# Kernel optimization log

Measured on AMD Instinct MI355X. Metric: run time of the kernel, lower is better.

The kernel has to match this reference:

```python
import jax, jax.numpy as jnp
import numpy as np

B, N = 4, 1024
DIM, DEPTH, HEADS, DHEAD, MLP = 512, 6, 8, 64, 2048
INNER = HEADS * DHEAD
SCALE = DHEAD ** -0.5
EPS = 1e-5


def setup_inputs() -> dict:
    key = jax.random.key(0)
    ks = jax.random.split(key, 16)
    w = lambda k, shape: (jax.random.normal(k, shape, jnp.float32) * 0.02)
    D = DEPTH
    return {
        "g": jax.random.normal(ks[0], (B, N, DIM), jnp.float32),
        "x": jax.random.normal(ks[1], (B, N, DIM), jnp.float32),
        # PreNorm + SelfAttention
        "ln1_s": jnp.ones((D, DIM)), "ln1_b": jnp.zeros((D, DIM)),
        "Wqkv": w(ks[2], (D, DIM, 3 * INNER)),
        "Wo_sa": w(ks[3], (D, INNER, DIM)), "bo_sa": jnp.zeros((D, DIM)),
        # RelationalCrossAttention
        "lng_s": jnp.ones((D, DIM)), "lng_b": jnp.zeros((D, DIM)),
        "lnx_s": jnp.ones((D, DIM)), "lnx_b": jnp.zeros((D, DIM)),
        "Wq": w(ks[4], (D, DIM, INNER)),
        "Wk": w(ks[5], (D, DIM, INNER)),
        "Wv": w(ks[6], (D, DIM, INNER)), "bv": jnp.zeros((D, INNER)),
        "Wo_ca": w(ks[7], (D, INNER, DIM)), "bo_ca": jnp.zeros((D, DIM)),
        # PreNorm + FeedForward (same module applied twice per layer)
        "lnf_s": jnp.ones((D, DIM)), "lnf_b": jnp.zeros((D, DIM)),
        "W1": w(ks[8], (D, DIM, MLP)), "b1": jnp.zeros((D, MLP)),
        "W2": w(ks[9], (D, MLP, DIM)), "b2": jnp.zeros((D, DIM)),
    }


def _ln(t, s, b):
    m = t.mean(-1, keepdims=True)
    v = ((t - m) ** 2).mean(-1, keepdims=True)
    return (t - m) / jnp.sqrt(v + EPS) * s + b


def _split_heads(t):  # [b, n, h*d] -> [b, h, n, d]
    b, n, _ = t.shape
    return t.reshape(b, n, HEADS, DHEAD).transpose(0, 2, 1, 3)


def _merge_heads(t):  # [b, h, n, d] -> [b, n, h*d]
    b, h, n, d = t.shape
    return t.transpose(0, 2, 1, 3).reshape(b, n, h * d)


def _attend(q, k, v):
    dots = jnp.einsum('bhnd,bhmd->bhnm', q, k) * SCALE
    attn = jax.nn.softmax(jnp.nan_to_num(dots, nan=-jnp.inf), axis=-1)
    attn = jnp.nan_to_num(attn)  # nan_to_num(0.0) post-softmax as in source
    return jnp.einsum('bhnm,bhmd->bhnd', attn, jnp.nan_to_num(v))


def reference(g, x, ln1_s, ln1_b, Wqkv, Wo_sa, bo_sa, lng_s, lng_b, lnx_s, lnx_b,
              Wq, Wk, Wv, bv, Wo_ca, bo_ca, lnf_s, lnf_b, W1, b1, W2, b2):
    for i in range(DEPTH):
        def ff(t):
            h = jax.nn.gelu(_ln(t, lnf_s[i], lnf_b[i]) @ W1[i] + b1[i], approximate=False)
            return h @ W2[i] + b2[i]
        # relational cross attention: q,k from g, v from x
        gn = _ln(g, lng_s[i], lng_b[i])
        xn = _ln(x, lnx_s[i], lnx_b[i])
        q = _split_heads(gn @ Wq[i])
        k = _split_heads(gn @ Wk[i])
        v = _split_heads(xn @ Wv[i] + bv[i])
        x = _merge_heads(_attend(q, k, v)) @ Wo_ca[i] + bo_ca[i] + x
        x = ff(x) + x
        # pre-norm self attention (skip connection enabled)
        sn = _ln(x, ln1_s[i], ln1_b[i])
        qkv = sn @ Wqkv[i]
        qs, ks_, vs = jnp.split(qkv, 3, axis=-1)
        sa = _merge_heads(_attend(_split_heads(qs), _split_heads(ks_), _split_heads(vs)))
        x = sa @ Wo_sa[i] + bo_sa[i] + x
        x = ff(x) + x
    return x
```

## Files before the change

### kernel.cpp

```cpp
#include <hip/hip_runtime.h>
#include <hip/hip_bf16.h>
#include <cstdint>
#include <cstddef>

#define DEV __device__ __forceinline__

using f32x4 = __attribute__((ext_vector_type(4))) float;
using bfx8  = __attribute__((ext_vector_type(8))) __bf16;
using s16x8 = __attribute__((ext_vector_type(8))) short;

DEV uint16_t f2bf(float f) {
    union { float f; uint32_t u; } x; x.f = f;
    uint32_t r = x.u + 0x7fffu + ((x.u >> 16) & 1u);
    return (uint16_t)(r >> 16);
}

DEV float gelu_exact(float v) {
    return 0.5f * v * (1.0f + erff(v * 0.70710678118654752f));
}

DEV f32x4 mfma16(s16x8 a, s16x8 b, f32x4 c) {
    return __builtin_amdgcn_mfma_f32_16x16x32_bf16(
        __builtin_bit_cast(bfx8, a), __builtin_bit_cast(bfx8, b), c, 0, 0, 0);
}

DEV void async_lds16(const void* g, void* l) {
    __builtin_amdgcn_global_load_lds(
        (const __attribute__((address_space(1))) uint32_t*)g,
        (__attribute__((address_space(3))) uint32_t*)l, 16, 0, 0);
}

template<int N> DEV void wait_vmcnt() {
    if constexpr (N == 0)      asm volatile("s_waitcnt vmcnt(0)" ::: "memory");
    else if constexpr (N == 4) asm volatile("s_waitcnt vmcnt(4)" ::: "memory");
    else static_assert(N == 0 || N == 4, "add vmcnt literal");
}
#define SBAR      asm volatile("s_barrier" ::: "memory")
#define LGKM0     asm volatile("s_waitcnt lgkmcnt(0)" ::: "memory")
#define SCHED0    __builtin_amdgcn_sched_barrier(0)

template<int HAS_SB>
__global__ __launch_bounds__(256)
void ln_t(const float* __restrict__ in, const float* __restrict__ sc,
          const float* __restrict__ bi, uint16_t* __restrict__ out)
{
    const int lane = threadIdx.x & 63;
    const size_t row = (size_t)blockIdx.x * 4 + (threadIdx.x >> 6);
    const float* p = in + row * 512 + lane * 8;
    float4 a = *(const float4*)p;
    float4 b4 = *(const float4*)(p + 4);
    float v[8] = {a.x, a.y, a.z, a.w, b4.x, b4.y, b4.z, b4.w};
    float s = 0.f, sq = 0.f;
#pragma unroll
    for (int j = 0; j < 8; ++j) { s += v[j]; sq += v[j] * v[j]; }
#pragma unroll
    for (int o = 1; o < 64; o <<= 1) { s += __shfl_xor(s, o); sq += __shfl_xor(sq, o); }
    const float mean = s * (1.0f / 512.0f);
    const float var  = sq * (1.0f / 512.0f) - mean * mean;
    const float rstd = rsqrtf(var + 1e-5f);
    const int c = lane * 8;
    uint16_t o8[8];
#pragma unroll
    for (int j = 0; j < 8; ++j) {
        float z = (v[j] - mean) * rstd;
        if (HAS_SB) z = z * sc[c + j] + bi[c + j];
        o8[j] = f2bf(z);
    }
    uint4 pk;
    pk.x = (uint32_t)o8[0] | ((uint32_t)o8[1] << 16);
    pk.y = (uint32_t)o8[2] | ((uint32_t)o8[3] << 16);
    pk.z = (uint32_t)o8[4] | ((uint32_t)o8[5] << 16);
    pk.w = (uint32_t)o8[6] | ((uint32_t)o8[7] << 16);
    *reinterpret_cast<uint4*>(out + row * 512 + c) = pk;
}

__global__ __launch_bounds__(256)
void wtrans(const float* __restrict__ W, uint16_t* __restrict__ WT, int K, int N,
            size_t lstride, int row0, const float* __restrict__ kscale)
{
    __shared__ float tile[32][33];
    const int l = blockIdx.z;
    const int k0 = blockIdx.x * 32, n0 = blockIdx.y * 32;
    const float* Wl = W + (size_t)l * K * N;
    uint16_t* WTl = WT + (size_t)l * lstride;
    const int tx = threadIdx.x, ty = threadIdx.y;
#pragma unroll
    for (int j = 0; j < 4; ++j) {
        const int k = k0 + ty + j * 8;
        float w = Wl[(size_t)k * N + n0 + tx];
        if (kscale) w *= kscale[l * K + k];
        tile[ty + j * 8][tx] = w;
    }
    __syncthreads();
#pragma unroll
    for (int j = 0; j < 4; ++j)
        WTl[(size_t)(row0 + n0 + ty + j * 8) * K + k0 + tx] = f2bf(tile[tx][ty + j * 8]);
}

__global__ __launch_bounds__(256)
void bfold(const float* __restrict__ b, const float* __restrict__ Wq,
           const float* __restrict__ Wk, float* __restrict__ out)
{
    const int n = blockIdx.x * 256 + threadIdx.x;
    const int l = blockIdx.y, sel = blockIdx.z;
    const float* bb = b + l * 512;
    const float* W = (sel ? Wk : Wq) + (size_t)l * 512 * 512;
    float s = 0.f;
    for (int k = 0; k < 512; ++k) s += bb[k] * W[(size_t)k * 512 + n];
    out[l * 1024 + sel * 512 + n] = s;
}

template<int BM, int BN, int NWR, int NWC, int MINW,
         int HAS_BIAS, int HAS_RESID, int DO_GELU, int OUT_BF16, int PARTIAL, int OUT_VT>
__global__ __launch_bounds__(NWR * NWC * 64, MINW)
void gemm6(const uint16_t* __restrict__ A, const uint16_t* __restrict__ BT,
           const float* __restrict__ bias, const float* __restrict__ resid,
           void* __restrict__ outp, uint16_t* __restrict__ vt,
           int M, int N, int K, int kh)
{
    constexpr int NT = NWR * NWC * 64;
    constexpr int WM = BM / NWR, WN = BN / NWC;
    constexpr int FM = WM / 16, FN = WN / 16;
    constexpr int ASLOTS = 8 * BM, BSLOTS = 8 * BN, TOT = ASLOTS + BSLOTS;
    constexpr int S = TOT / NT;
    static_assert(S == 4, "vmcnt literal assumes S==4");
    __shared__ uint16_t As[2][ASLOTS * 8];
    __shared__ uint16_t Bs[2][BSLOTS * 8];
    const int tid = threadIdx.x, lane = tid & 63;
    const int w = tid >> 6, wr = w / NWC, wc = w % NWC;
    const int kg = lane >> 4, lr = lane & 15;
    const int nwg = gridDim.x;
    const int id0 = blockIdx.x;
    const int id = (id0 & 7) * (nwg >> 3) + (id0 >> 3);
    const int nbn = N / BN;
    const size_t m0 = (size_t)(id / nbn) * BM;
    const size_t n0 = (size_t)(id % nbn) * BN;
    const int kbase = PARTIAL ? blockIdx.y * kh : 0;

    auto stage = [&](int b, int k0) {
#pragma unroll
        for (int j = 0; j < S; ++j) {
            const int s = j * NT + tid;
            if (s < ASLOTS) {
                const int sub = s / BM, row = s % BM;
                async_lds16(A + (m0 + row) * K + k0 + sub * 8, &As[b][s * 8]);
            } else {
                const int s2 = s - ASLOTS;
                const int sub = s2 / BN, row = s2 % BN;
                async_lds16(BT + (n0 + row) * K + k0 + sub * 8, &Bs[b][s2 * 8]);
            }
        }
    };

    f32x4 acc[FM][FN] = {};
    const int nt = kh / 64;
    stage(0, kbase);
    stage(1, kbase + 64);
    int cur = 0;
    for (int t = 0; t < nt; ++t) {
        if (t < nt - 1) wait_vmcnt<S>(); else wait_vmcnt<0>();
        SBAR;
        s16x8 af[2][FM], bf[2][FN];
#pragma unroll
        for (int ks = 0; ks < 2; ++ks) {
#pragma unroll
            for (int i = 0; i < FM; ++i)
                af[ks][i] = *(const s16x8*)&As[cur][((ks * 4 + kg) * BM + wr * WM + i * 16 + lr) * 8];
#pragma unroll
            for (int j = 0; j < FN; ++j)
                bf[ks][j] = *(const s16x8*)&Bs[cur][((ks * 4 + kg) * BN + wc * WN + j * 16 + lr) * 8];
        }
        __builtin_amdgcn_s_setprio(1);
#pragma unroll
        for (int ks = 0; ks < 2; ++ks)
#pragma unroll
            for (int i = 0; i < FM; ++i)
#pragma unroll
                for (int j = 0; j < FN; ++j)
                    acc[i][j] = mfma16(af[ks][i], bf[ks][j], acc[i][j]);
        __builtin_amdgcn_s_setprio(0);
        LGKM0; SCHED0;
        SBAR;
        if (t + 2 < nt) stage(cur, kbase + (t + 2) * 64);
        cur ^= 1;
    }
    if (OUT_VT == 1 || (OUT_VT == 2 && n0 >= 1024)) {
#pragma unroll
        for (int i = 0; i < FM; ++i) {
            const size_t rbase = m0 + wr * WM + i * 16 + kg * 4;
            const int b = (int)(rbase >> 10), nloc = (int)(rbase & 1023);
#pragma unroll
            for (int j = 0; j < FN; ++j) {
                const int col = (int)n0 + wc * WN + j * 16 + lr;
                const int c2 = (OUT_VT == 2) ? col - 1024 : col;
                const float bval = HAS_BIAS ? bias[c2] : 0.0f;
                const int h = c2 >> 6, d = c2 & 63;
                ushort4 pk;
                pk.x = f2bf(acc[i][j][0] + bval);
                pk.y = f2bf(acc[i][j][1] + bval);
                pk.z = f2bf(acc[i][j][2] + bval);
                pk.w = f2bf(acc[i][j][3] + bval);
                *(ushort4*)&vt[((size_t)(b * 8 + h) * 64 + d) * 1024 + nloc] = pk;
            }
        }
        return;
    }
    float* pout = PARTIAL ? (float*)outp + (size_t)blockIdx.y * M * (size_t)N : nullptr;
#pragma unroll
    for (int i = 0; i < FM; ++i) {
        const size_t rbase = m0 + wr * WM + i * 16 + kg * 4;
#pragma unroll
        for (int j = 0; j < FN; ++j) {
            const size_t col = n0 + wc * WN + j * 16 + lr;
            const float bval = HAS_BIAS ? bias[col] : 0.0f;
#pragma unroll
            for (int r = 0; r < 4; ++r) {
                const size_t row = rbase + r;
                float v = acc[i][j][r] + bval;
                if (PARTIAL) { pout[row * (size_t)N + col] = v; continue; }
                if (DO_GELU)  v = gelu_exact(v);
                if (HAS_RESID) v += resid[row * (size_t)N + col];
                if (OUT_BF16) ((uint16_t*)outp)[row * (size_t)N + col] = f2bf(v);
                else          ((float*)outp)[row * (size_t)N + col] = v;
            }
        }
    }
}

template<int DO_LN>
__global__ __launch_bounds__(256)
void reduce_ln(const float* __restrict__ p, const float* __restrict__ bias,
               float* __restrict__ x, const float* __restrict__ sc,
               const float* __restrict__ bi, uint16_t* __restrict__ xn)
{
    const int lane = threadIdx.x & 63;
    const size_t row = (size_t)blockIdx.x * 4 + (threadIdx.x >> 6);
    const int c = lane * 8;
    const size_t off = row * 512 + c;
    const float* p0 = p + off;
    const float* p1 = p + 4096ull * 512 + off;
    float4 a0 = *(const float4*)p0,        a1 = *(const float4*)(p0 + 4);
    float4 b0 = *(const float4*)p1,        b1 = *(const float4*)(p1 + 4);
    float4 s0 = *(const float4*)(bias + c), s1 = *(const float4*)(bias + c + 4);
    float4 r0 = *(const float4*)(x + off), r1 = *(const float4*)(x + off + 4);
    float v[8];
    v[0] = a0.x + b0.x + s0.x + r0.x;  v[1] = a0.y + b0.y + s0.y + r0.y;
    v[2] = a0.z + b0.z + s0.z + r0.z;  v[3] = a0.w + b0.w + s0.w + r0.w;
    v[4] = a1.x + b1.x + s1.x + r1.x;  v[5] = a1.y + b1.y + s1.y + r1.y;
    v[6] = a1.z + b1.z + s1.z + r1.z;  v[7] = a1.w + b1.w + s1.w + r1.w;
    *(float4*)(x + off)     = make_float4(v[0], v[1], v[2], v[3]);
    *(float4*)(x + off + 4) = make_float4(v[4], v[5], v[6], v[7]);
    if (DO_LN) {
        float s = 0.f, sq = 0.f;
#pragma unroll
        for (int j = 0; j < 8; ++j) { s += v[j]; sq += v[j] * v[j]; }
#pragma unroll
        for (int o = 1; o < 64; o <<= 1) { s += __shfl_xor(s, o); sq += __shfl_xor(sq, o); }
        const float mean = s * (1.0f / 512.0f);
        const float var  = sq * (1.0f / 512.0f) - mean * mean;
        const float rstd = rsqrtf(var + 1e-5f);
        uint16_t o8[8];
#pragma unroll
        for (int j = 0; j < 8; ++j)
            o8[j] = f2bf((v[j] - mean) * rstd * sc[c + j] + bi[c + j]);
        uint4 pk;
        pk.x = (uint32_t)o8[0] | ((uint32_t)o8[1] << 16);
        pk.y = (uint32_t)o8[2] | ((uint32_t)o8[3] << 16);
        pk.z = (uint32_t)o8[4] | ((uint32_t)o8[5] << 16);
        pk.w = (uint32_t)o8[6] | ((uint32_t)o8[7] << 16);
        *reinterpret_cast<uint4*>(xn + off) = pk;
    }
}

__global__ __launch_bounds__(256)
void attn_flash(const uint16_t* __restrict__ Qb, const uint16_t* __restrict__ Kb,
                const uint16_t* __restrict__ Vt, uint16_t* __restrict__ Ob,
                int qstride, int kstride, int qoff, int koff)
{
    __shared__ uint16_t Ks[2][4096];
    __shared__ uint16_t Vs[2][4096];
    __shared__ uint16_t Pb[4][1024];
    const int tid = threadIdx.x, lane = tid & 63, w = tid >> 6;
    const int kg = lane >> 4, lr = lane & 15;
    const int bh = blockIdx.y, b = bh >> 3, h = bh & 7;
    const int q0 = blockIdx.x * 64;
    const float CEXP = 0.125f * 1.44269504f;

    s16x8 aq0, aq1;
    {
        const size_t qrow = (size_t)b * 1024 + q0 + w * 16 + lr;
        const uint16_t* qp = Qb + qrow * qstride + qoff + h * 64 + kg * 8;
        aq0 = *(const s16x8*)qp;
        aq1 = *(const s16x8*)(qp + 32);
    }
    const uint16_t* kbase = Kb + (size_t)b * 1024 * kstride + koff + h * 64;
    const uint16_t* vbase = Vt + (size_t)bh * 65536;

    float l_r[4] = {0.f, 0.f, 0.f, 0.f};
    f32x4 acc[4] = {};

    auto stage = [&](int buf, int kv0) {
#pragma unroll
        for (int j = 0; j < 2; ++j) {
            const int s = j * 256 + tid;
            const int sub = s >> 6, row = s & 63;
            async_lds16(kbase + (size_t)(kv0 + row) * kstride + sub * 8, &Ks[buf][s * 8]);
            async_lds16(vbase + (size_t)row * 1024 + kv0 + sub * 8,      &Vs[buf][s * 8]);
        }
    };

    stage(0, 0);
    __syncthreads();
    int cur = 0;
    for (int t = 0; t < 16; ++t) {
        if (t < 15) stage(cur ^ 1, (t + 1) * 64);
        f32x4 s4[4];
        __builtin_amdgcn_s_setprio(1);
#pragma unroll
        for (int ni = 0; ni < 4; ++ni) {
            s16x8 bk0 = *(const s16x8*)&Ks[cur][(kg * 64 + ni * 16 + lr) * 8];
            s16x8 bk1 = *(const s16x8*)&Ks[cur][((4 + kg) * 64 + ni * 16 + lr) * 8];
            f32x4 z = {};
            z = mfma16(aq0, bk0, z);
            z = mfma16(aq1, bk1, z);
            s4[ni] = z;
        }
        __builtin_amdgcn_s_setprio(0);
#pragma unroll
        for (int ni = 0; ni < 4; ++ni) {
            const int slotb = (ni * 2 + (lr >> 3)) * 16 + kg * 4;
#pragma unroll
            for (int r = 0; r < 4; ++r) {
                const float pe = __builtin_amdgcn_exp2f(s4[ni][r] * CEXP);
                l_r[r] += pe;
                Pb[w][(slotb + r) * 8 + (lr & 7)] = f2bf(pe);
            }
        }
        s16x8 ap0 = *(const s16x8*)&Pb[w][(kg * 16 + lr) * 8];
        s16x8 ap1 = *(const s16x8*)&Pb[w][((4 + kg) * 16 + lr) * 8];
        __builtin_amdgcn_s_setprio(1);
#pragma unroll
        for (int ni = 0; ni < 4; ++ni) {
            s16x8 bv0 = *(const s16x8*)&Vs[cur][(kg * 64 + ni * 16 + lr) * 8];
            s16x8 bv1 = *(const s16x8*)&Vs[cur][((4 + kg) * 64 + ni * 16 + lr) * 8];
            acc[ni] = mfma16(ap0, bv0, acc[ni]);
            acc[ni] = mfma16(ap1, bv1, acc[ni]);
        }
        __builtin_amdgcn_s_setprio(0);
        __syncthreads();
        cur ^= 1;
    }
    float linv[4];
#pragma unroll
    for (int r = 0; r < 4; ++r) {
        float l = l_r[r];
        l += __shfl_xor(l, 1); l += __shfl_xor(l, 2);
        l += __shfl_xor(l, 4); l += __shfl_xor(l, 8);
        linv[r] = 1.0f / l;
    }
#pragma unroll
    for (int ni = 0; ni < 4; ++ni)
#pragma unroll
        for (int r = 0; r < 4; ++r) {
            const float v = acc[ni][r] * linv[r];
            const size_t row = (size_t)b * 1024 + q0 + w * 16 + kg * 4 + r;
            Ob[row * 512 + h * 64 + ni * 16 + lr] = f2bf(v);
        }
}

extern "C" void kernel_launch(void* const* d_in, const int* in_sizes, int n_in,
                              void* d_out, int out_size, void* d_ws, size_t ws_size,
                              hipStream_t stream)
{
    (void)in_sizes; (void)n_in; (void)out_size; (void)ws_size;
    const float* g     = (const float*)d_in[0];
    const float* x0    = (const float*)d_in[1];
    const float* ln1_s = (const float*)d_in[2];
    const float* ln1_b = (const float*)d_in[3];
    const float* Wqkv  = (const float*)d_in[4];
    const float* Wo_sa = (const float*)d_in[5];
    const float* bo_sa = (const float*)d_in[6];
    const float* lng_s = (const float*)d_in[7];
    const float* lng_b = (const float*)d_in[8];
    const float* lnx_s = (const float*)d_in[9];
    const float* lnx_b = (const float*)d_in[10];
    const float* Wq    = (const float*)d_in[11];
    const float* Wk    = (const float*)d_in[12];
    const float* Wv    = (const float*)d_in[13];
    const float* bv    = (const float*)d_in[14];
    const float* Wo_ca = (const float*)d_in[15];
    const float* bo_ca = (const float*)d_in[16];
    const float* lnf_s = (const float*)d_in[17];
    const float* lnf_b = (const float*)d_in[18];
    const float* W1    = (const float*)d_in[19];
    const float* b1    = (const float*)d_in[20];
    const float* W2    = (const float*)d_in[21];
    const float* b2    = (const float*)d_in[22];

    float* x = (float*)d_out;

    char* p = (char*)d_ws;
    auto carve = [&](size_t n) { char* r = p; p += (n + 255) & ~(size_t)255; return r; };
    uint16_t* WqkT  = (uint16_t*)carve(6ull * 1024 * 512 * 2);
    uint16_t* WvT   = (uint16_t*)carve(6ull * 512 * 512 * 2);
    uint16_t* WocaT = (uint16_t*)carve(6ull * 512 * 512 * 2);
    uint16_t* WqkvT = (uint16_t*)carve(6ull * 1536 * 512 * 2);
    uint16_t* WosaT = (uint16_t*)carve(6ull * 512 * 512 * 2);
    uint16_t* W1T   = (uint16_t*)carve(6ull * 2048 * 512 * 2);
    uint16_t* W2T   = (uint16_t*)carve(6ull * 512 * 2048 * 2);
    float*    bqk   = (float*)carve(6144ull * 4);
    uint16_t* zg    = (uint16_t*)carve(4096ull * 512 * 2);
    uint16_t* qkall = (uint16_t*)carve(4096ull * 6144 * 2);
    uint16_t* xn    = (uint16_t*)carve(4096ull * 512 * 2);
    uint16_t* qkvu  = (uint16_t*)carve(4096ull * 1536 * 2);
    uint16_t* vt    = (uint16_t*)carve(32ull * 64 * 1024 * 2);
    uint16_t* ab    = (uint16_t*)carve(4096ull * 512 * 2);
    uint16_t* hb    = (uint16_t*)carve(4096ull * 2048 * 2);
    float*    pk2   = (float*)carve(2ull * 4096 * 512 * 4);

    dim3 tb(32, 8);
    wtrans<<<dim3(16, 16, 6), tb, 0, stream>>>(Wq,    WqkT,  512, 512,  1024ull * 512, 0,   lng_s);
    wtrans<<<dim3(16, 16, 6), tb, 0, stream>>>(Wk,    WqkT,  512, 512,  1024ull * 512, 512, lng_s);
    wtrans<<<dim3(16, 16, 6), tb, 0, stream>>>(Wv,    WvT,   512, 512,  512ull * 512, 0, nullptr);
    wtrans<<<dim3(16, 16, 6), tb, 0, stream>>>(Wo_ca, WocaT, 512, 512,  512ull * 512, 0, nullptr);
    wtrans<<<dim3(16, 48, 6), tb, 0, stream>>>(Wqkv,  WqkvT, 512, 1536, 1536ull * 512, 0, nullptr);
    wtrans<<<dim3(16, 16, 6), tb, 0, stream>>>(Wo_sa, WosaT, 512, 512,  512ull * 512, 0, nullptr);
    wtrans<<<dim3(16, 64, 6), tb, 0, stream>>>(W1,    W1T,   512, 2048, 2048ull * 512, 0, nullptr);
    wtrans<<<dim3(64, 16, 6), tb, 0, stream>>>(W2,    W2T,   2048, 512, 2048ull * 512, 0, nullptr);
    bfold<<<dim3(2, 6, 2), 256, 0, stream>>>(lng_b, Wq, Wk, bqk);

    hipMemcpyAsync(x, x0, 4096ull * 512 * 4, hipMemcpyDeviceToDevice, stream);

    ln_t<0><<<1024, 256, 0, stream>>>(g, nullptr, nullptr, zg);
    ln_t<1><<<1024, 256, 0, stream>>>(x, lnx_s, lnx_b, xn);
    gemm6<128, 128, 2, 4, 4, 1, 0, 0, 1, 0, 0><<<1536, 512, 0, stream>>>(
        zg, WqkT, bqk, nullptr, qkall, nullptr, 4096, 6144, 512, 512);

    const dim3 ga(16, 32);

    for (int l = 0; l < 6; ++l) {
        const size_t o512 = (size_t)l * 512, oW = (size_t)l * 512 * 512;
        const size_t oW1 = (size_t)l * 2048 * 512, oWqkv = (size_t)l * 1536 * 512;
        const size_t o2048 = (size_t)l * 2048;

        gemm6<64, 64, 2, 2, 4, 1, 0, 0, 0, 0, 1><<<512, 256, 0, stream>>>(
            xn, WvT + oW, bv + o512, nullptr, nullptr, vt, 4096, 512, 512, 512);
        attn_flash<<<ga, 256, 0, stream>>>(qkall, qkall, vt, ab, 6144, 6144,
                                           l * 1024, l * 1024 + 512);
        gemm6<64, 64, 2, 2, 4, 1, 1, 0, 0, 0, 0><<<512, 256, 0, stream>>>(
            ab, WocaT + oW, bo_ca + o512, x, x, nullptr, 4096, 512, 512, 512);

        ln_t<1><<<1024, 256, 0, stream>>>(x, lnf_s + o512, lnf_b + o512, xn);
        gemm6<128, 128, 2, 4, 4, 1, 0, 1, 1, 0, 0><<<512, 512, 0, stream>>>(
            xn, W1T + oW1, b1 + o2048, nullptr, hb, nullptr, 4096, 2048, 512, 512);
        gemm6<64, 64, 2, 2, 4, 0, 0, 0, 0, 1, 0><<<dim3(512, 2), 256, 0, stream>>>(
            hb, W2T + oW1, nullptr, nullptr, pk2, nullptr, 4096, 512, 2048, 1024);
        reduce_ln<1><<<1024, 256, 0, stream>>>(pk2, b2 + o512, x,
                                               ln1_s + o512, ln1_b + o512, xn);

        gemm6<128, 128, 2, 4, 4, 0, 0, 0, 1, 0, 2><<<384, 512, 0, stream>>>(
            xn, WqkvT + oWqkv, nullptr, nullptr, qkvu, vt, 4096, 1536, 512, 512);
        attn_flash<<<ga, 256, 0, stream>>>(qkvu, qkvu, vt, ab, 1536, 1536, 0, 512);
        gemm6<64, 64, 2, 2, 4, 1, 1, 0, 0, 0, 0><<<512, 256, 0, stream>>>(
            ab, WosaT + oW, bo_sa + o512, x, x, nullptr, 4096, 512, 512, 512);

        ln_t<1><<<1024, 256, 0, stream>>>(x, lnf_s + o512, lnf_b + o512, xn);
        gemm6<128, 128, 2, 4, 4, 1, 0, 1, 1, 0, 0><<<512, 512, 0, stream>>>(
            xn, W1T + oW1, b1 + o2048, nullptr, hb, nullptr, 4096, 2048, 512, 512);
        gemm6<64, 64, 2, 2, 4, 0, 0, 0, 0, 1, 0><<<dim3(512, 2), 256, 0, stream>>>(
            hb, W2T + oW1, nullptr, nullptr, pk2, nullptr, 4096, 512, 2048, 1024);
        if (l < 5)
            reduce_ln<1><<<1024, 256, 0, stream>>>(pk2, b2 + o512, x,
                                                   lnx_s + o512 + 512, lnx_b + o512 + 512, xn);
        else
            reduce_ln<0><<<1024, 256, 0, stream>>>(pk2, b2 + o512, x,
                                                   nullptr, nullptr, nullptr);
    }
}
```

Before: 1.649 ms.

## Drop split-K for W2 GEMM and remap tiles to XCD-local rectangles

```diff
diff --git a/kernel.cpp b/kernel.cpp
--- a/kernel.cpp
+++ b/kernel.cpp
@@ -111,12 +111,12 @@
 }
 
 template<int BM, int BN, int NWR, int NWC, int MINW,
-         int HAS_BIAS, int HAS_RESID, int DO_GELU, int OUT_BF16, int PARTIAL, int OUT_VT>
+         int HAS_BIAS, int HAS_RESID, int DO_GELU, int OUT_BF16, int OUT_VT>
 __global__ __launch_bounds__(NWR * NWC * 64, MINW)
-void gemm6(const uint16_t* __restrict__ A, const uint16_t* __restrict__ BT,
+void gemm7(const uint16_t* __restrict__ A, const uint16_t* __restrict__ BT,
            const float* __restrict__ bias, const float* __restrict__ resid,
            void* __restrict__ outp, uint16_t* __restrict__ vt,
-           int M, int N, int K, int kh)
+           int M, int N, int K)
 {
     constexpr int NT = NWR * NWC * 64;
     constexpr int WM = BM / NWR, WN = BN / NWC;
@@ -129,13 +129,13 @@
     const int tid = threadIdx.x, lane = tid & 63;
     const int w = tid >> 6, wr = w / NWC, wc = w % NWC;
     const int kg = lane >> 4, lr = lane & 15;
-    const int nwg = gridDim.x;
-    const int id0 = blockIdx.x;
-    const int id = (id0 & 7) * (nwg >> 3) + (id0 >> 3);
-    const int nbn = N / BN;
-    const size_t m0 = (size_t)(id / nbn) * BM;
-    const size_t n0 = (size_t)(id % nbn) * BN;
-    const int kbase = PARTIAL ? blockIdx.y * kh : 0;
+    const int nbn = N / BN, nbm = M / BM;
+    const int rect_m = nbm >> 1, rect_n = nbn >> 2;
+    const int xcd = blockIdx.x & 7, c = blockIdx.x >> 3;
+    const int bm = (xcd >> 2) * rect_m + c / rect_n;
+    const int bn = (xcd & 3) * rect_n + c % rect_n;
+    const size_t m0 = (size_t)bm * BM;
+    const size_t n0 = (size_t)bn * BN;
 
     auto stage = [&](int b, int k0) {
 #pragma unroll
@@ -153,9 +153,9 @@
     };
 
     f32x4 acc[FM][FN] = {};
-    const int nt = kh / 64;
-    stage(0, kbase);
-    stage(1, kbase + 64);
+    const int nt = K / 64;
+    stage(0, 0);
+    stage(1, 64);
     int cur = 0;
     for (int t = 0; t < nt; ++t) {
         if (t < nt - 1) wait_vmcnt<S>(); else wait_vmcnt<0>();
@@ -181,7 +181,7 @@
         __builtin_amdgcn_s_setprio(0);
         LGKM0; SCHED0;
         SBAR;
-        if (t + 2 < nt) stage(cur, kbase + (t + 2) * 64);
+        if (t + 2 < nt) stage(cur, (t + 2) * 64);
         cur ^= 1;
     }
     if (OUT_VT == 1 || (OUT_VT == 2 && n0 >= 1024)) {
@@ -205,7 +205,6 @@
         }
         return;
     }
-    float* pout = PARTIAL ? (float*)outp + (size_t)blockIdx.y * M * (size_t)N : nullptr;
 #pragma unroll
     for (int i = 0; i < FM; ++i) {
         const size_t rbase = m0 + wr * WM + i * 16 + kg * 4;
@@ -217,58 +216,12 @@
             for (int r = 0; r < 4; ++r) {
                 const size_t row = rbase + r;
                 float v = acc[i][j][r] + bval;
-                if (PARTIAL) { pout[row * (size_t)N + col] = v; continue; }
                 if (DO_GELU)  v = gelu_exact(v);
                 if (HAS_RESID) v += resid[row * (size_t)N + col];
                 if (OUT_BF16) ((uint16_t*)outp)[row * (size_t)N + col] = f2bf(v);
                 else          ((float*)outp)[row * (size_t)N + col] = v;
             }
         }
-    }
-}
-
-template<int DO_LN>
-__global__ __launch_bounds__(256)
-void reduce_ln(const float* __restrict__ p, const float* __restrict__ bias,
-               float* __restrict__ x, const float* __restrict__ sc,
-               const float* __restrict__ bi, uint16_t* __restrict__ xn)
-{
-    const int lane = threadIdx.x & 63;
-    const size_t row = (size_t)blockIdx.x * 4 + (threadIdx.x >> 6);
-    const int c = lane * 8;
-    const size_t off = row * 512 + c;
-    const float* p0 = p + off;
-    const float* p1 = p + 4096ull * 512 + off;
-    float4 a0 = *(const float4*)p0,        a1 = *(const float4*)(p0 + 4);
-    float4 b0 = *(const float4*)p1,        b1 = *(const float4*)(p1 + 4);
-    float4 s0 = *(const float4*)(bias + c), s1 = *(const float4*)(bias + c + 4);
-    float4 r0 = *(const float4*)(x + off), r1 = *(const float4*)(x + off + 4);
-    float v[8];
-    v[0] = a0.x + b0.x + s0.x + r0.x;  v[1] = a0.y + b0.y + s0.y + r0.y;
-    v[2] = a0.z + b0.z + s0.z + r0.z;  v[3] = a0.w + b0.w + s0.w + r0.w;
-    v[4] = a1.x + b1.x + s1.x + r1.x;  v[5] = a1.y + b1.y + s1.y + r1.y;
-    v[6] = a1.z + b1.z + s1.z + r1.z;  v[7] = a1.w + b1.w + s1.w + r1.w;
-    *(float4*)(x + off)     = make_float4(v[0], v[1], v[2], v[3]);
-    *(float4*)(x + off + 4) = make_float4(v[4], v[5], v[6], v[7]);
-    if (DO_LN) {
-        float s = 0.f, sq = 0.f;
-#pragma unroll
-        for (int j = 0; j < 8; ++j) { s += v[j]; sq += v[j] * v[j]; }
-#pragma unroll
-        for (int o = 1; o < 64; o <<= 1) { s += __shfl_xor(s, o); sq += __shfl_xor(sq, o); }
-        const float mean = s * (1.0f / 512.0f);
-        const float var  = sq * (1.0f / 512.0f) - mean * mean;
-        const float rstd = rsqrtf(var + 1e-5f);
-        uint16_t o8[8];
-#pragma unroll
-        for (int j = 0; j < 8; ++j)
-            o8[j] = f2bf((v[j] - mean) * rstd * sc[c + j] + bi[c + j]);
-        uint4 pk;
-        pk.x = (uint32_t)o8[0] | ((uint32_t)o8[1] << 16);
-        pk.y = (uint32_t)o8[2] | ((uint32_t)o8[3] << 16);
-        pk.z = (uint32_t)o8[4] | ((uint32_t)o8[5] << 16);
-        pk.w = (uint32_t)o8[6] | ((uint32_t)o8[7] << 16);
-        *reinterpret_cast<uint4*>(xn + off) = pk;
     }
 }
 
@@ -416,7 +369,6 @@
     uint16_t* vt    = (uint16_t*)carve(32ull * 64 * 1024 * 2);
     uint16_t* ab    = (uint16_t*)carve(4096ull * 512 * 2);
     uint16_t* hb    = (uint16_t*)carve(4096ull * 2048 * 2);
-    float*    pk2   = (float*)carve(2ull * 4096 * 512 * 4);
 
     dim3 tb(32, 8);
     wtrans<<<dim3(16, 16, 6), tb, 0, stream>>>(Wq,    WqkT,  512, 512,  1024ull * 512, 0,   lng_s);
@@ -433,8 +385,8 @@
 
     ln_t<0><<<1024, 256, 0, stream>>>(g, nullptr, nullptr, zg);
     ln_t<1><<<1024, 256, 0, stream>>>(x, lnx_s, lnx_b, xn);
-    gemm6<128, 128, 2, 4, 4, 1, 0, 0, 1, 0, 0><<<1536, 512, 0, stream>>>(
-        zg, WqkT, bqk, nullptr, qkall, nullptr, 4096, 6144, 512, 512);
+    gemm7<128, 128, 2, 4, 4, 1, 0, 0, 1, 0><<<1536, 512, 0, stream>>>(
+        zg, WqkT, bqk, nullptr, qkall, nullptr, 4096, 6144, 512);
 
     const dim3 ga(16, 32);
 
@@ -443,37 +395,32 @@
         const size_t oW1 = (size_t)l * 2048 * 512, oWqkv = (size_t)l * 1536 * 512;
         const size_t o2048 = (size_t)l * 2048;
 
-        gemm6<64, 64, 2, 2, 4, 1, 0, 0, 0, 0, 1><<<512, 256, 0, stream>>>(
-            xn, WvT + oW, bv + o512, nullptr, nullptr, vt, 4096, 512, 512, 512);
+        gemm7<64, 64, 2, 2, 4, 1, 0, 0, 0, 1><<<512, 256, 0, stream>>>(
+            xn, WvT + oW, bv + o512, nullptr, nullptr, vt, 4096, 512, 512);
         attn_flash<<<ga, 256, 0, stream>>>(qkall, qkall, vt, ab, 6144, 6144,
                                            l * 1024, l * 1024 + 512);
-        gemm6<64, 64, 2, 2, 4, 1, 1, 0, 0, 0, 0><<<512, 256, 0, stream>>>(
-            ab, WocaT + oW, bo_ca + o512, x, x, nullptr, 4096, 512, 512, 512);
+        gemm7<64, 64, 2, 2, 4, 1, 1, 0, 0, 0><<<512, 256, 0, stream>>>(
+            ab, WocaT + oW, bo_ca + o512, x, x, nullptr, 4096, 512, 512);
 
         ln_t<1><<<1024, 256, 0, stream>>>(x, lnf_s + o512, lnf_b + o512, xn);
-        gemm6<128, 128, 2, 4, 4, 1, 0, 1, 1, 0, 0><<<512, 512, 0, stream>>>(
-            xn, W1T + oW1, b1 + o2048, nullptr, hb, nullptr, 4096, 2048, 512, 512);
-        gemm6<64, 64, 2, 2, 4, 0, 0, 0, 0, 1, 0><<<dim3(512, 2), 256, 0, stream>>>(
-            hb, W2T + oW1, nullptr, nullptr, pk2, nullptr, 4096, 512, 2048, 1024);
-        reduce_ln<1><<<1024, 256, 0, stream>>>(pk2, b2 + o512, x,
-                                               ln1_s + o512, ln1_b + o512, xn);
-
-        gemm6<128, 128, 2, 4, 4, 0, 0, 0, 1, 0, 2><<<384, 512, 0, stream>>>(
-            xn, WqkvT + oWqkv, nullptr, nullptr, qkvu, vt, 4096, 1536, 512, 512);
+        gemm7<128, 128, 2, 4, 4, 1, 0, 1, 1, 0><<<512, 512, 0, stream>>>(
+            xn, W1T + oW1, b1 + o2048, nullptr, hb, nullptr, 4096, 2048, 512);
+        gemm7<64, 64, 2, 2, 4, 1, 1, 0, 0, 0><<<512, 256, 0, stream>>>(
+            hb, W2T + oW1, b2 + o512, x, x, nullptr, 4096, 512, 2048);
+        ln_t<1><<<1024, 256, 0, stream>>>(x, ln1_s + o512, ln1_b + o512, xn);
+
+        gemm7<128, 128, 2, 4, 4, 0, 0, 0, 1, 2><<<384, 512, 0, stream>>>(
+            xn, WqkvT + oWqkv, nullptr, nullptr, qkvu, vt, 4096, 1536, 512);
         attn_flash<<<ga, 256, 0, stream>>>(qkvu, qkvu, vt, ab, 1536, 1536, 0, 512);
-        gemm6<64, 64, 2, 2, 4, 1, 1, 0, 0, 0, 0><<<512, 256, 0, stream>>>(
-            ab, WosaT + oW, bo_sa + o512, x, x, nullptr, 4096, 512, 512, 512);
+        gemm7<64, 64, 2, 2, 4, 1, 1, 0, 0, 0><<<512, 256, 0, stream>>>(
+            ab, WosaT + oW, bo_sa + o512, x, x, nullptr, 4096, 512, 512);
 
         ln_t<1><<<1024, 256, 0, stream>>>(x, lnf_s + o512, lnf_b + o512, xn);
-        gemm6<128, 128, 2, 4, 4, 1, 0, 1, 1, 0, 0><<<512, 512, 0, stream>>>(
-            xn, W1T + oW1, b1 + o2048, nullptr, hb, nullptr, 4096, 2048, 512, 512);
-        gemm6<64, 64, 2, 2, 4, 0, 0, 0, 0, 1, 0><<<dim3(512, 2), 256, 0, stream>>>(
-            hb, W2T + oW1, nullptr, nullptr, pk2, nullptr, 4096, 512, 2048, 1024);
+        gemm7<128, 128, 2, 4, 4, 1, 0, 1, 1, 0><<<512, 512, 0, stream>>>(
+            xn, W1T + oW1, b1 + o2048, nullptr, hb, nullptr, 4096, 2048, 512);
+        gemm7<64, 64, 2, 2, 4, 1, 1, 0, 0, 0><<<512, 256, 0, stream>>>(
+            hb, W2T + oW1, b2 + o512, x, x, nullptr, 4096, 512, 2048);
         if (l < 5)
-            reduce_ln<1><<<1024, 256, 0, stream>>>(pk2, b2 + o512, x,
-                                                   lnx_s + o512 + 512, lnx_b + o512 + 512, xn);
-        else
-            reduce_ln<0><<<1024, 256, 0, stream>>>(pk2, b2 + o512, x,
-                                                   nullptr, nullptr, nullptr);
-    }
-}
+            ln_t<1><<<1024, 256, 0, stream>>>(x, lnx_s + o512 + 512, lnx_b + o512 + 512, xn);
+    }
+}
```

Result: faster. 1.591 ms (-3.5%).
